# Kernel tuning notes

Hardware: AMD Instinct MI355X
Metric: run time of the kernel (lower is better)

Reference implementation:

```python
import jax, jax.numpy as jnp
import numpy as np

HEAD_NUM = 8
EMB_SIZE = 768
B, N = 8, 1024


def setup_inputs() -> dict:
    key = jax.random.key(0)
    ks = jax.random.split(key, 9)
    s = 0.02
    return {
        "x": jax.random.normal(ks[0], (B, N, EMB_SIZE), dtype=jnp.float32),
        "Wq": jax.random.normal(ks[1], (EMB_SIZE, EMB_SIZE), dtype=jnp.float32) * s,
        "bq": jax.random.normal(ks[2], (EMB_SIZE,), dtype=jnp.float32) * s,
        "Wk": jax.random.normal(ks[3], (EMB_SIZE, EMB_SIZE), dtype=jnp.float32) * s,
        "bk": jax.random.normal(ks[4], (EMB_SIZE,), dtype=jnp.float32) * s,
        "Wv": jax.random.normal(ks[5], (EMB_SIZE, EMB_SIZE), dtype=jnp.float32) * s,
        "bv": jax.random.normal(ks[6], (EMB_SIZE,), dtype=jnp.float32) * s,
        "Wp": jax.random.normal(ks[7], (EMB_SIZE, EMB_SIZE), dtype=jnp.float32) * s,
        "bp": jax.random.normal(ks[8], (EMB_SIZE,), dtype=jnp.float32) * s,
    }


def reference(x, Wq, bq, Wk, bk, Wv, bv, Wp, bp):
    b, n, e = x.shape
    h = HEAD_NUM
    d = e // h
    # nn.Linear: y = x @ W^T + b
    q = (x @ Wq.T + bq).reshape(b, h, n, d)  # NOTE: raw reshape, as in source
    k = (x @ Wk.T + bk).reshape(b, h, n, d)
    v = (x @ Wv.T + bv).reshape(b, h, n, d)
    energy = jnp.einsum('bhqd,bhkd->bhqk', q, k)
    # source divides by sqrt(emb_size) AFTER softmax (faithful)
    attn = jax.nn.softmax(energy, axis=-1) / jnp.sqrt(jnp.float32(e))
    out = jnp.einsum('bhql,bhld->bhqd', attn, v).reshape(b, n, h * d)
    return out @ Wp.T + bp
```

## Files before the change

kernel.cpp:

```cpp
#include <hip/hip_runtime.h>
#include <hip/hip_bf16.h>


typedef __attribute__((ext_vector_type(8))) short short8;
typedef __attribute__((ext_vector_type(4))) float floatx4;
typedef __attribute__((ext_vector_type(16))) float floatx16;

static constexpr int EMB = 768;
static constexpr int SEQ = 1024;
static constexpr int DH = 96;
static constexpr int NBH = 64;
static constexpr int HEADBLK = SEQ * DH;
static constexpr int MROWS = 8192;
static constexpr int NW = EMB * EMB;
static constexpr int QKVN = 3 * EMB;

__device__ __forceinline__ unsigned bfround(float f) {
    unsigned u = __builtin_bit_cast(unsigned, f);
    return u + 0x7FFFu + ((u >> 16) & 1u);
}
__device__ __forceinline__ unsigned short f2bf(float f) {
    return (unsigned short)(bfround(f) >> 16);
}
__device__ __forceinline__ unsigned pk2(float lo, float hi) {
    return (bfround(lo) >> 16) | (bfround(hi) & 0xFFFF0000u);
}

__device__ __forceinline__ void gload16(const unsigned short* g, unsigned short* l) {
    __builtin_amdgcn_global_load_lds(
        (const __attribute__((address_space(1))) unsigned int*)g,
        (__attribute__((address_space(3))) unsigned int*)l, 16, 0, 0);
}

__global__ void cast_all(const float* __restrict__ x,
                         const float* __restrict__ Wq, const float* __restrict__ Wk,
                         const float* __restrict__ Wv, const float* __restrict__ Wp,
                         const float* __restrict__ bq, const float* __restrict__ bk,
                         const float* __restrict__ bv,
                         unsigned short* __restrict__ xb,
                         unsigned short* __restrict__ Wqkv, unsigned short* __restrict__ Wpb,
                         float* __restrict__ bias) {
    int bx = blockIdx.x;
    if (bx < 6144) {
        int i = bx * 1024 + threadIdx.x * 4;
        float4 v = *reinterpret_cast<const float4*>(x + i);
        ushort4 o;
        o.x = f2bf(v.x); o.y = f2bf(v.y); o.z = f2bf(v.z); o.w = f2bf(v.w);
        *reinterpret_cast<ushort4*>(xb + i) = o;
    } else if (bx < 8448) {
        int i4 = (bx - 6144) * 1024 + threadIdx.x * 4;
        const float* src;
        unsigned short* dst;
        if (i4 < 3 * NW) {
            int wi = i4 / NW;
            src = (wi == 0) ? Wq + i4 : (wi == 1) ? Wk + (i4 - NW) : Wv + (i4 - 2 * NW);
            dst = Wqkv + i4;
        } else {
            src = Wp + (i4 - 3 * NW);
            dst = Wpb + (i4 - 3 * NW);
        }
        float4 v = *reinterpret_cast<const float4*>(src);
        ushort4 o;
        o.x = f2bf(v.x); o.y = f2bf(v.y); o.z = f2bf(v.z); o.w = f2bf(v.w);
        *reinterpret_cast<ushort4*>(dst) = o;
    } else {
        int j = (bx - 8448) * 256 + threadIdx.x;
        if (j < QKVN)
            bias[j] = (j < 768) ? bq[j] : (j < 1536) ? bk[j - 768] : bv[j - 1536];
    }
}

__global__ __launch_bounds__(256) void gemm_qkv(
    const unsigned short* __restrict__ A,
    const unsigned short* __restrict__ Bm,
    const float* __restrict__ bias,
    unsigned short* __restrict__ Qo,
    unsigned short* __restrict__ Ko,
    unsigned short* __restrict__ Vo) {
    __shared__ unsigned short As[128 * 64];
    __shared__ unsigned short Bs[128 * 64];
    const int K = EMB;

    const int t = threadIdx.x;
    const int lane = t & 63;
    const int w = t >> 6;
    const int wm = (w >> 1) * 64;
    const int wn = (w & 1) * 64;
    const int l32 = lane & 31;
    const int lh = lane >> 5;
    const int bm = blockIdx.x * 128;
    const int by = blockIdx.y;
    const int bn = by * 128;

    const unsigned short* Agp[4];
    const unsigned short* Bgp[4];
#pragma unroll
    for (int i = 0; i < 4; i++) {
        int f = i * 2048 + w * 512 + lane * 8;
        int row = f >> 6;
        int cc = (f >> 3) & 7;
        int gk = (cc ^ (row & 7)) * 8;
        Agp[i] = A + (size_t)(bm + row) * K + gk;
        Bgp[i] = Bm + (size_t)(bn + row) * K + gk;
    }

    floatx16 acc[2][2];
#pragma unroll
    for (int i = 0; i < 2; i++)
#pragma unroll
        for (int j = 0; j < 2; j++)
#pragma unroll
            for (int r = 0; r < 16; r++) acc[i][j][r] = 0.0f;

    const int sx = lane & 7;
    for (int k0 = 0; k0 < K; k0 += 64) {
        __syncthreads();
#pragma unroll
        for (int i = 0; i < 4; i++) {
            gload16(Agp[i] + k0, As + i * 2048 + w * 512);
            gload16(Bgp[i] + k0, Bs + i * 2048 + w * 512);
        }
        __syncthreads();

#pragma unroll
        for (int ks = 0; ks < 4; ks++) {
            const int co = ((ks * 2 + lh) ^ sx) * 8;
            short8 af[2], bfr[2];
#pragma unroll
            for (int mt = 0; mt < 2; mt++)
                af[mt] = *reinterpret_cast<const short8*>(As + (wm + mt * 32 + l32) * 64 + co);
#pragma unroll
            for (int nt = 0; nt < 2; nt++)
                bfr[nt] = *reinterpret_cast<const short8*>(Bs + (wn + nt * 32 + l32) * 64 + co);
#pragma unroll
            for (int mt = 0; mt < 2; mt++)
#pragma unroll
                for (int nt = 0; nt < 2; nt++)
                    acc[mt][nt] = __builtin_amdgcn_mfma_f32_32x32x16_bf16(af[mt], bfr[nt], acc[mt][nt], 0, 0, 0);
        }
    }

    unsigned short* dst = (by < 6) ? Qo : (by < 12) ? Ko : Vo;
    const int bnl = (by % 6) * 128;
#pragma unroll
    for (int mt = 0; mt < 2; mt++) {
#pragma unroll
        for (int nt = 0; nt < 2; nt++) {
            int colg = bn + wn + nt * 32 + l32;
            int coll = bnl + wn + nt * 32 + l32;
            float bb = bias[colg];
#pragma unroll
            for (int rg = 0; rg < 4; rg++) {
                int rowb = bm + wm + mt * 32 + rg * 8 + lh * 4;
#pragma unroll
                for (int rr = 0; rr < 4; rr++)
                    dst[(size_t)(rowb + rr) * EMB + coll] = f2bf(acc[mt][nt][rg * 4 + rr] + bb);
            }
        }
    }
}

__global__ __launch_bounds__(256) void gemm_proj(
    const unsigned short* __restrict__ A,
    const unsigned short* __restrict__ Bm,
    const float* __restrict__ bias,
    float* __restrict__ C) {
    __shared__ unsigned short As[64 * 64];
    __shared__ unsigned short Bs[128 * 64];
    const int K = EMB, N = EMB;

    const int t = threadIdx.x;
    const int lane = t & 63;
    const int w = t >> 6;
    const int wm = (w >> 1) * 32;
    const int wn = (w & 1) * 64;
    const int l32 = lane & 31;
    const int lh = lane >> 5;
    const int bm = blockIdx.x * 64;
    const int bn = blockIdx.y * 128;

    const unsigned short* Agp[2];
    const unsigned short* Bgp[4];
#pragma unroll
    for (int i = 0; i < 2; i++) {
        int f = i * 2048 + w * 512 + lane * 8;
        int row = f >> 6;
        int cc = (f >> 3) & 7;
        Agp[i] = A + (size_t)(bm + row) * K + ((cc ^ (row & 7)) * 8);
    }
#pragma unroll
    for (int i = 0; i < 4; i++) {
        int f = i * 2048 + w * 512 + lane * 8;
        int row = f >> 6;
        int cc = (f >> 3) & 7;
        Bgp[i] = Bm + (size_t)(bn + row) * K + ((cc ^ (row & 7)) * 8);
    }

    floatx16 acc[2];
#pragma unroll
    for (int j = 0; j < 2; j++)
#pragma unroll
        for (int r = 0; r < 16; r++) acc[j][r] = 0.0f;

    const int sx = lane & 7;
    for (int k0 = 0; k0 < K; k0 += 64) {
        __syncthreads();
#pragma unroll
        for (int i = 0; i < 2; i++) gload16(Agp[i] + k0, As + i * 2048 + w * 512);
#pragma unroll
        for (int i = 0; i < 4; i++) gload16(Bgp[i] + k0, Bs + i * 2048 + w * 512);
        __syncthreads();

#pragma unroll
        for (int ks = 0; ks < 4; ks++) {
            const int co = ((ks * 2 + lh) ^ sx) * 8;
            short8 af = *reinterpret_cast<const short8*>(As + (wm + l32) * 64 + co);
            short8 bfr[2];
#pragma unroll
            for (int nt = 0; nt < 2; nt++)
                bfr[nt] = *reinterpret_cast<const short8*>(Bs + (wn + nt * 32 + l32) * 64 + co);
#pragma unroll
            for (int nt = 0; nt < 2; nt++)
                acc[nt] = __builtin_amdgcn_mfma_f32_32x32x16_bf16(af, bfr[nt], acc[nt], 0, 0, 0);
        }
    }

#pragma unroll
    for (int nt = 0; nt < 2; nt++) {
        int col = bn + wn + nt * 32 + l32;
        float bb = bias[col];
#pragma unroll
        for (int rg = 0; rg < 4; rg++) {
            int rowb = bm + wm + rg * 8 + lh * 4;
#pragma unroll
            for (int rr = 0; rr < 4; rr++)
                C[(size_t)(rowb + rr) * N + col] = acc[nt][rg * 4 + rr] + bb;
        }
    }
}

__global__ __launch_bounds__(256) void transpose_v(const unsigned short* __restrict__ V,
                                                   unsigned short* __restrict__ Vt) {
    __shared__ unsigned short L[64 * 104];
    const int t = threadIdx.x;
    const int bh = blockIdx.x, nb = blockIdx.y;
    const unsigned short* Vg = V + (size_t)bh * HEADBLK + (size_t)nb * 64 * DH;
#pragma unroll
    for (int i = 0; i < 3; i++) {
        int f = i * 2048 + t * 8;
        int r = f / 96, c = f - r * 96;
        *reinterpret_cast<short8*>(L + r * 104 + c) = *reinterpret_cast<const short8*>(Vg + f);
    }
    __syncthreads();
    unsigned short* dst = Vt + (size_t)bh * HEADBLK;
#pragma unroll
    for (int i = 0; i < 3; i++) {
        int f = i * 2048 + t * 8;
        int d = f >> 6, c = f & 63;
        int base = (c & 32) + ((c >> 3) & 3) * 4;
        union { short8 s; unsigned short u[8]; } o;
#pragma unroll
        for (int j = 0; j < 8; j++) {
            int key = base + ((j & 4) << 2) + (j & 3);
            o.u[j] = L[key * 104 + d];
        }
        *reinterpret_cast<short8*>(dst + d * SEQ + nb * 64 + c) = o.s;
    }
}

__global__ __launch_bounds__(256) void attn_kernel(
    const unsigned short* __restrict__ Q,
    const unsigned short* __restrict__ K,
    const unsigned short* __restrict__ Vt,
    unsigned short* __restrict__ O) {
    __shared__ unsigned short Qs[128 * 104];
    __shared__ unsigned short Ks[64 * 104];
    __shared__ unsigned short Vs[96 * 72];

    const int t = threadIdx.x;
    const int lane = t & 63;
    const int w = t >> 6;
    const int lrow = lane & 15;
    const int quad = lane >> 4;
    const int bh = blockIdx.x, qb = blockIdx.y;

    const unsigned short* Qh = Q + (size_t)bh * HEADBLK;
    const unsigned short* Kh = K + (size_t)bh * HEADBLK;
    const unsigned short* Vth = Vt + (size_t)bh * HEADBLK;

    const unsigned short* Kp[3];
    const unsigned short* Vp[3];
    unsigned short* KsW[3];
    unsigned short* VsW[3];
#pragma unroll
    for (int i = 0; i < 3; i++) {
        int f = i * 2048 + t * 8;
        int r = f / 96, c = f - r * 96;
        Kp[i] = Kh + f;
        KsW[i] = Ks + r * 104 + c;
        int d = f >> 6, cv = f & 63;
        Vp[i] = Vth + d * SEQ + cv;
        VsW[i] = Vs + d * 72 + cv;
    }

    short8 kreg[3], vreg[3];
#pragma unroll
    for (int i = 0; i < 3; i++) {
        kreg[i] = *reinterpret_cast<const short8*>(Kp[i]);
        vreg[i] = *reinterpret_cast<const short8*>(Vp[i]);
    }

    {
        const unsigned short* src = Qh + (size_t)qb * 128 * DH;
#pragma unroll
        for (int i = 0; i < 6; i++) {
            int f = i * 2048 + t * 8;
            int r = f / 96, c = f - r * 96;
            *reinterpret_cast<short8*>(Qs + r * 104 + c) = *reinterpret_cast<const short8*>(src + f);
        }
    }

    float l_[2] = {0.0f, 0.0f};
    floatx4 acco[2][6];
#pragma unroll
    for (int qt = 0; qt < 2; qt++)
#pragma unroll
        for (int n = 0; n < 6; n++)
#pragma unroll
            for (int r = 0; r < 4; r++) acco[qt][n][r] = 0.0f;

    for (int kb = 0; kb < 16; kb++) {
        __syncthreads();
#pragma unroll
        for (int i = 0; i < 3; i++) {
            *reinterpret_cast<short8*>(KsW[i]) = kreg[i];
            *reinterpret_cast<short8*>(VsW[i]) = vreg[i];
        }
        __syncthreads();
        if (kb < 15) {
#pragma unroll
            for (int i = 0; i < 3; i++) {
                kreg[i] = *reinterpret_cast<const short8*>(Kp[i] + (kb + 1) * 6144);
                vreg[i] = *reinterpret_cast<const short8*>(Vp[i] + (kb + 1) * 64);
            }
        }

#pragma unroll
        for (int qt = 0; qt < 2; qt++) {
            floatx4 sacc[4];
#pragma unroll
            for (int kt = 0; kt < 4; kt++)
#pragma unroll
                for (int r = 0; r < 4; r++) sacc[kt][r] = 0.0f;
#pragma unroll
            for (int ks = 0; ks < 3; ks++) {
                short8 bq = *reinterpret_cast<const short8*>(
                    Qs + (w * 32 + qt * 16 + lrow) * 104 + ks * 32 + quad * 8);
#pragma unroll
                for (int kt = 0; kt < 4; kt++) {
                    short8 ak = *reinterpret_cast<const short8*>(
                        Ks + (kt * 16 + lrow) * 104 + ks * 32 + quad * 8);
                    sacc[kt] = __builtin_amdgcn_mfma_f32_16x16x32_bf16(ak, bq, sacc[kt], 0, 0, 0);
                }
            }

            float rs = 0.0f;
            unsigned pk01[4], pk23[4];
#pragma unroll
            for (int kt = 0; kt < 4; kt++) {
                float p0 = __expf(sacc[kt][0]);
                float p1 = __expf(sacc[kt][1]);
                float p2 = __expf(sacc[kt][2]);
                float p3 = __expf(sacc[kt][3]);
                rs += (p0 + p1) + (p2 + p3);
                pk01[kt] = pk2(p0, p1);
                pk23[kt] = pk2(p2, p3);
            }
            rs += __shfl_xor(rs, 16);
            rs += __shfl_xor(rs, 32);
            l_[qt] += rs;

#pragma unroll
            for (int s = 0; s < 2; s++) {
                union { short8 s8; unsigned u[4]; } bp;
                bp.u[0] = pk01[2 * s];
                bp.u[1] = pk23[2 * s];
                bp.u[2] = pk01[2 * s + 1];
                bp.u[3] = pk23[2 * s + 1];
#pragma unroll
                for (int n = 0; n < 6; n++) {
                    short8 av = *reinterpret_cast<const short8*>(
                        Vs + (n * 16 + lrow) * 72 + s * 32 + quad * 8);
                    acco[qt][n] = __builtin_amdgcn_mfma_f32_16x16x32_bf16(av, bp.s8, acco[qt][n], 0, 0, 0);
                }
            }
        }
    }

    const float inv_sqrt_e = 0.036084391824351615f;
#pragma unroll
    for (int qt = 0; qt < 2; qt++) {
        float invl = inv_sqrt_e / l_[qt];
        unsigned short* dst = O + (size_t)bh * HEADBLK +
                              (size_t)(qb * 128 + w * 32 + qt * 16 + lrow) * DH;
#pragma unroll
        for (int n = 0; n < 6; n++) {
            uint2 o2;
            o2.x = pk2(acco[qt][n][0] * invl, acco[qt][n][1] * invl);
            o2.y = pk2(acco[qt][n][2] * invl, acco[qt][n][3] * invl);
            *reinterpret_cast<uint2*>(dst + n * 16 + quad * 4) = o2;
        }
    }
}

extern "C" void kernel_launch(void* const* d_in, const int* in_sizes, int n_in,
                              void* d_out, int out_size, void* d_ws, size_t ws_size,
                              hipStream_t stream) {
    const float* x = (const float*)d_in[0];
    const float* Wq = (const float*)d_in[1];
    const float* bq = (const float*)d_in[2];
    const float* Wk = (const float*)d_in[3];
    const float* bk = (const float*)d_in[4];
    const float* Wv = (const float*)d_in[5];
    const float* bv = (const float*)d_in[6];
    const float* Wp = (const float*)d_in[7];
    const float* bp = (const float*)d_in[8];
    float* out = (float*)d_out;

    char* ws = (char*)d_ws;
    size_t off = 0;
    auto alloc = [&](size_t bytes) {
        char* p = ws + off;
        off += (bytes + 255) & ~(size_t)255;
        return p;
    };
    const int nx = MROWS * EMB;
    unsigned short* xb    = (unsigned short*)alloc((size_t)nx * 2);
    unsigned short* Wqkvb = (unsigned short*)alloc((size_t)3 * NW * 2);
    unsigned short* Wpb   = (unsigned short*)alloc((size_t)NW * 2);
    float*          biasq = (float*)alloc((size_t)QKVN * 4);
    unsigned short* Qb    = (unsigned short*)alloc((size_t)nx * 2);
    unsigned short* Kb    = (unsigned short*)alloc((size_t)nx * 2);
    unsigned short* Vb    = (unsigned short*)alloc((size_t)nx * 2);
    unsigned short* Vtb   = (unsigned short*)alloc((size_t)nx * 2);
    unsigned short* Ob    = (unsigned short*)alloc((size_t)nx * 2);

    cast_all<<<8457, 256, 0, stream>>>(x, Wq, Wk, Wv, Wp, bq, bk, bv,
                                       xb, Wqkvb, Wpb, biasq);

    gemm_qkv<<<dim3(MROWS / 128, QKVN / 128), 256, 0, stream>>>(
        xb, Wqkvb, biasq, Qb, Kb, Vb);

    transpose_v<<<dim3(NBH, SEQ / 64), 256, 0, stream>>>(Vb, Vtb);

    attn_kernel<<<dim3(NBH, SEQ / 128), 256, 0, stream>>>(Qb, Kb, Vtb, Ob);

    gemm_proj<<<dim3(MROWS / 64, EMB / 128), 256, 0, stream>>>(Ob, Wpb, bp, out);
}
```

Baseline: 190.2 us.

## Halve attention query tile and keep Q fragments in registers

```diff
diff --git a/kernel.cpp b/kernel.cpp
--- a/kernel.cpp
+++ b/kernel.cpp
@@ -268,12 +268,11 @@
     }
 }
 
-__global__ __launch_bounds__(256) void attn_kernel(
+__global__ __launch_bounds__(256, 4) void attn_kernel(
     const unsigned short* __restrict__ Q,
     const unsigned short* __restrict__ K,
     const unsigned short* __restrict__ Vt,
     unsigned short* __restrict__ O) {
-    __shared__ unsigned short Qs[128 * 104];
     __shared__ unsigned short Ks[64 * 104];
     __shared__ unsigned short Vs[96 * 72];
 
@@ -287,6 +286,14 @@
     const unsigned short* Qh = Q + (size_t)bh * HEADBLK;
     const unsigned short* Kh = K + (size_t)bh * HEADBLK;
     const unsigned short* Vth = Vt + (size_t)bh * HEADBLK;
+
+    short8 qf[3];
+    {
+        const unsigned short* qsrc = Qh + (size_t)(qb * 64 + w * 16 + lrow) * DH + quad * 8;
+#pragma unroll
+        for (int ks = 0; ks < 3; ks++)
+            qf[ks] = *reinterpret_cast<const short8*>(qsrc + ks * 32);
+    }
 
     const unsigned short* Kp[3];
     const unsigned short* Vp[3];
@@ -310,24 +317,12 @@
         vreg[i] = *reinterpret_cast<const short8*>(Vp[i]);
     }
 
-    {
-        const unsigned short* src = Qh + (size_t)qb * 128 * DH;
-#pragma unroll
-        for (int i = 0; i < 6; i++) {
-            int f = i * 2048 + t * 8;
-            int r = f / 96, c = f - r * 96;
-            *reinterpret_cast<short8*>(Qs + r * 104 + c) = *reinterpret_cast<const short8*>(src + f);
-        }
-    }
-
-    float l_[2] = {0.0f, 0.0f};
-    floatx4 acco[2][6];
-#pragma unroll
-    for (int qt = 0; qt < 2; qt++)
-#pragma unroll
-        for (int n = 0; n < 6; n++)
-#pragma unroll
-            for (int r = 0; r < 4; r++) acco[qt][n][r] = 0.0f;
+    float l_ = 0.0f;
+    floatx4 acco[6];
+#pragma unroll
+    for (int n = 0; n < 6; n++)
+#pragma unroll
+        for (int r = 0; r < 4; r++) acco[n][r] = 0.0f;
 
     for (int kb = 0; kb < 16; kb++) {
         __syncthreads();
@@ -345,71 +340,63 @@
             }
         }
 
-#pragma unroll
-        for (int qt = 0; qt < 2; qt++) {
-            floatx4 sacc[4];
-#pragma unroll
-            for (int kt = 0; kt < 4; kt++)
-#pragma unroll
-                for (int r = 0; r < 4; r++) sacc[kt][r] = 0.0f;
-#pragma unroll
-            for (int ks = 0; ks < 3; ks++) {
-                short8 bq = *reinterpret_cast<const short8*>(
-                    Qs + (w * 32 + qt * 16 + lrow) * 104 + ks * 32 + quad * 8);
-#pragma unroll
-                for (int kt = 0; kt < 4; kt++) {
-                    short8 ak = *reinterpret_cast<const short8*>(
-                        Ks + (kt * 16 + lrow) * 104 + ks * 32 + quad * 8);
-                    sacc[kt] = __builtin_amdgcn_mfma_f32_16x16x32_bf16(ak, bq, sacc[kt], 0, 0, 0);
-                }
+        floatx4 sacc[4];
+#pragma unroll
+        for (int kt = 0; kt < 4; kt++)
+#pragma unroll
+            for (int r = 0; r < 4; r++) sacc[kt][r] = 0.0f;
+#pragma unroll
+        for (int ks = 0; ks < 3; ks++) {
+#pragma unroll
+            for (int kt = 0; kt < 4; kt++) {
+                short8 ak = *reinterpret_cast<const short8*>(
+                    Ks + (kt * 16 + lrow) * 104 + ks * 32 + quad * 8);
+                sacc[kt] = __builtin_amdgcn_mfma_f32_16x16x32_bf16(ak, qf[ks], sacc[kt], 0, 0, 0);
             }
-
-            float rs = 0.0f;
-            unsigned pk01[4], pk23[4];
-#pragma unroll
-            for (int kt = 0; kt < 4; kt++) {
-                float p0 = __expf(sacc[kt][0]);
-                float p1 = __expf(sacc[kt][1]);
-                float p2 = __expf(sacc[kt][2]);
-                float p3 = __expf(sacc[kt][3]);
-                rs += (p0 + p1) + (p2 + p3);
-                pk01[kt] = pk2(p0, p1);
-                pk23[kt] = pk2(p2, p3);
+        }
+
+        float rs = 0.0f;
+        unsigned pk01[4], pk23[4];
+#pragma unroll
+        for (int kt = 0; kt < 4; kt++) {
+            float p0 = __expf(sacc[kt][0]);
+            float p1 = __expf(sacc[kt][1]);
+            float p2 = __expf(sacc[kt][2]);
+            float p3 = __expf(sacc[kt][3]);
+            rs += (p0 + p1) + (p2 + p3);
+            pk01[kt] = pk2(p0, p1);
+            pk23[kt] = pk2(p2, p3);
+        }
+        rs += __shfl_xor(rs, 16);
+        rs += __shfl_xor(rs, 32);
+        l_ += rs;
+
+#pragma unroll
+        for (int s = 0; s < 2; s++) {
+            union { short8 s8; unsigned u[4]; } bp;
+            bp.u[0] = pk01[2 * s];
+            bp.u[1] = pk23[2 * s];
+            bp.u[2] = pk01[2 * s + 1];
+            bp.u[3] = pk23[2 * s + 1];
+#pragma unroll
+            for (int n = 0; n < 6; n++) {
+                short8 av = *reinterpret_cast<const short8*>(
+                    Vs + (n * 16 + lrow) * 72 + s * 32 + quad * 8);
+                acco[n] = __builtin_amdgcn_mfma_f32_16x16x32_bf16(av, bp.s8, acco[n], 0, 0, 0);
             }
-            rs += __shfl_xor(rs, 16);
-            rs += __shfl_xor(rs, 32);
-            l_[qt] += rs;
-
-#pragma unroll
-            for (int s = 0; s < 2; s++) {
-                union { short8 s8; unsigned u[4]; } bp;
-                bp.u[0] = pk01[2 * s];
-                bp.u[1] = pk23[2 * s];
-                bp.u[2] = pk01[2 * s + 1];
-                bp.u[3] = pk23[2 * s + 1];
-#pragma unroll
-                for (int n = 0; n < 6; n++) {
-                    short8 av = *reinterpret_cast<const short8*>(
-                        Vs + (n * 16 + lrow) * 72 + s * 32 + quad * 8);
-                    acco[qt][n] = __builtin_amdgcn_mfma_f32_16x16x32_bf16(av, bp.s8, acco[qt][n], 0, 0, 0);
-                }
-            }
         }
     }
 
     const float inv_sqrt_e = 0.036084391824351615f;
-#pragma unroll
-    for (int qt = 0; qt < 2; qt++) {
-        float invl = inv_sqrt_e / l_[qt];
-        unsigned short* dst = O + (size_t)bh * HEADBLK +
-                              (size_t)(qb * 128 + w * 32 + qt * 16 + lrow) * DH;
-#pragma unroll
-        for (int n = 0; n < 6; n++) {
-            uint2 o2;
-            o2.x = pk2(acco[qt][n][0] * invl, acco[qt][n][1] * invl);
-            o2.y = pk2(acco[qt][n][2] * invl, acco[qt][n][3] * invl);
-            *reinterpret_cast<uint2*>(dst + n * 16 + quad * 4) = o2;
-        }
+    float invl = inv_sqrt_e / l_;
+    unsigned short* dst = O + (size_t)bh * HEADBLK +
+                          (size_t)(qb * 64 + w * 16 + lrow) * DH;
+#pragma unroll
+    for (int n = 0; n < 6; n++) {
+        uint2 o2;
+        o2.x = pk2(acco[n][0] * invl, acco[n][1] * invl);
+        o2.y = pk2(acco[n][2] * invl, acco[n][3] * invl);
+        *reinterpret_cast<uint2*>(dst + n * 16 + quad * 4) = o2;
     }
 }
 
@@ -453,7 +440,7 @@
 
     transpose_v<<<dim3(NBH, SEQ / 64), 256, 0, stream>>>(Vb, Vtb);
 
-    attn_kernel<<<dim3(NBH, SEQ / 128), 256, 0, stream>>>(Qb, Kb, Vtb, Ob);
+    attn_kernel<<<dim3(NBH, SEQ / 64), 256, 0, stream>>>(Qb, Kb, Vtb, Ob);
 
     gemm_proj<<<dim3(MROWS / 64, EMB / 128), 256, 0, stream>>>(Ob, Wpb, bp, out);
 }
```

Result: slower. 194.3 us (+2.1%).
